# Kernel tuning notes

Measured on AMD Instinct MI355X. Metric: run time of the kernel, lower is better.

Reference implementation:

```python
import jax, jax.numpy as jnp
import numpy as np

N = 100000
E = 1600000
IN_CH = 32
HID = 64
HEADS = 2
NUM_CLASSES = 12
NEG_SLOPE = 0.2


def gat_conv(x, src, dst, W, a_src, a_dst, bias, concat):
    """PyG-style GATConv (self-loops already appended to src/dst).
    x: [N, F_in], W: [F_in, H*C], a_src/a_dst: [H, C], bias: [H*C] or [C]."""
    n = x.shape[0]
    h = (x @ W).reshape(n, HEADS, -1)                    # [N, H, C]
    al_s = jnp.einsum('nhc,hc->nh', h, a_src)            # [N, H]
    al_d = jnp.einsum('nhc,hc->nh', h, a_dst)            # [N, H]
    e = jax.nn.leaky_relu(al_s[src] + al_d[dst], NEG_SLOPE)  # [Etot, H]
    # segment softmax over destination neighborhoods
    e_max = jax.ops.segment_max(e, dst, num_segments=n)      # [N, H]
    ex = jnp.exp(e - e_max[dst])                              # [Etot, H]
    denom = jax.ops.segment_sum(ex, dst, num_segments=n)     # [N, H]
    alpha = ex / denom[dst]                                   # [Etot, H]
    msg = h[src] * alpha[:, :, None]                          # [Etot, H, C]
    out = jax.ops.segment_sum(msg, dst, num_segments=n)      # [N, H, C]
    if concat:
        out = out.reshape(n, -1)
    else:
        out = out.mean(axis=1)
    return out + bias


def prelu(x, a):
    return jnp.where(x >= 0, x, a * x)


def setup_inputs() -> dict:
    key = jax.random.key(0)
    ks = jax.random.split(key, 16)
    HC = HEADS * HID
    d = {
        'x': jax.random.normal(ks[0], (N, IN_CH), jnp.float32),
        'edge_index': jax.random.randint(ks[1], (2, E), 0, N, jnp.int32),
        'W1': jax.random.normal(ks[2], (IN_CH, HC), jnp.float32) * 0.1,
        'a1s': jax.random.normal(ks[3], (HEADS, HID), jnp.float32) * 0.1,
        'a1d': jax.random.normal(ks[4], (HEADS, HID), jnp.float32) * 0.1,
        'b1': jnp.zeros((HC,), jnp.float32),
        'W2': jax.random.normal(ks[5], (HC, HC), jnp.float32) * 0.1,
        'a2s': jax.random.normal(ks[6], (HEADS, HID), jnp.float32) * 0.1,
        'a2d': jax.random.normal(ks[7], (HEADS, HID), jnp.float32) * 0.1,
        'b2': jnp.zeros((HC,), jnp.float32),
        'W3': jax.random.normal(ks[8], (HC, HC), jnp.float32) * 0.1,
        'a3s': jax.random.normal(ks[9], (HEADS, HID), jnp.float32) * 0.1,
        'a3d': jax.random.normal(ks[10], (HEADS, HID), jnp.float32) * 0.1,
        'b3': jnp.zeros((HID,), jnp.float32),
        'prelu_a': jnp.float32(0.25),
        'Wc': jax.random.normal(ks[11], (HID, NUM_CLASSES), jnp.float32) * 0.1,
        'bc': jnp.zeros((NUM_CLASSES,), jnp.float32),
    }
    return d


def reference(x, edge_index, W1, a1s, a1d, b1, W2, a2s, a2d, b2,
              W3, a3s, a3d, b3, prelu_a, Wc, bc):
    loops = jnp.arange(N, dtype=edge_index.dtype)
    src = jnp.concatenate([edge_index[0], loops])
    dst = jnp.concatenate([edge_index[1], loops])
    h = gat_conv(x, src, dst, W1, a1s, a1d, b1, concat=True)
    h = prelu(h, prelu_a)
    h = gat_conv(h, src, dst, W2, a2s, a2d, b2, concat=True)
    h = prelu(h, prelu_a)
    h = gat_conv(h, src, dst, W3, a3s, a3d, b3, concat=False)
    h = prelu(h, prelu_a)
    return h @ Wc + bc
```

## Files before the change

### kernel.cpp

```cpp
#include <hip/hip_runtime.h>
#include <stdint.h>

#define NN 100000
#define NE 1600000
#define ET (NE + NN)
#define HC 128
#define HID 64
#define NCLS 12
#define BSZ 512
#define NBK ((NN + BSZ - 1) / BSZ)
#define CHUNK 8192
#define NPB ((ET + CHUNK - 1) / CHUNK)

typedef _Float16 f16;
typedef _Float16 f16x2 __attribute__((ext_vector_type(2)));
typedef _Float16 f16x4 __attribute__((ext_vector_type(4)));
typedef _Float16 f16x8 __attribute__((ext_vector_type(8)));
typedef float f32x4 __attribute__((ext_vector_type(4)));

__global__ __launch_bounds__(256) void k_hist(const int* __restrict__ ei, int* __restrict__ hgrid) {
    __shared__ int h[NBK];
    int tid = threadIdx.x;
    for (int b = tid; b < NBK; b += 256) h[b] = 0;
    __syncthreads();
    long base = (long)blockIdx.x * CHUNK;
#pragma unroll
    for (int k = 0; k < CHUNK / 256; k++) {
        long i = base + k * 256 + tid;
        if (i < ET) {
            int d = (i < NE) ? ei[NE + i] : (int)(i - NE);
            atomicAdd(&h[d >> 9], 1);
        }
    }
    __syncthreads();
    for (int b = tid; b < NBK; b += 256) hgrid[blockIdx.x * NBK + b] = h[b];
}

__global__ __launch_bounds__(256) void k_bscan(int* __restrict__ hgrid,
                                               int* __restrict__ bucketStart,
                                               int* __restrict__ rp) {
    __shared__ int s[256];
    int tid = threadIdx.x;
    int tot = 0;
    if (tid < NBK)
        for (int b = 0; b < NPB; b++) tot += hgrid[b * NBK + tid];
    s[tid] = tot;
    __syncthreads();
    for (int o = 1; o < 256; o <<= 1) {
        int t = (tid >= o) ? s[tid - o] : 0;
        __syncthreads();
        s[tid] += t;
        __syncthreads();
    }
    int excl = s[tid] - tot;
    if (tid < NBK) {
        bucketStart[tid] = excl;
        int run = excl;
        for (int b = 0; b < NPB; b++) {
            int t = hgrid[b * NBK + tid];
            hgrid[b * NBK + tid] = run;
            run += t;
        }
    }
    if (tid == 0) { bucketStart[NBK] = ET; rp[NN] = ET; }
}

__global__ __launch_bounds__(256) void k_part(const int* __restrict__ ei,
                                              const int* __restrict__ hgrid,
                                              uint32_t* __restrict__ ebuf) {
    __shared__ int h[NBK];
    __shared__ int base[NBK];
    int tid = threadIdx.x;
    for (int b = tid; b < NBK; b += 256) {
        base[b] = hgrid[blockIdx.x * NBK + b];
        h[b] = 0;
    }
    __syncthreads();
    long cbase = (long)blockIdx.x * CHUNK;
#pragma unroll
    for (int k = 0; k < CHUNK / 256; k++) {
        long i = cbase + k * 256 + tid;
        if (i < ET) {
            int s, d;
            if (i < NE) { s = ei[i]; d = ei[NE + i]; } else { s = d = (int)(i - NE); }
            int bk = d >> 9;
            int off = atomicAdd(&h[bk], 1);
            ebuf[base[bk] + off] = (uint32_t)s | ((uint32_t)(d & 511) << 17);
        }
    }
}

__global__ __launch_bounds__(512) void k_build(const uint32_t* __restrict__ ebuf,
                                               const int* __restrict__ bucketStart,
                                               int* __restrict__ rp, int* __restrict__ colx) {
    __shared__ int cnt[BSZ];
    __shared__ int fill[BSZ];
    int b = blockIdx.x, tid = threadIdx.x;
    int e0 = bucketStart[b], e1 = bucketStart[b + 1], m = e1 - e0;
    cnt[tid] = 0;
    __syncthreads();
    for (int k = tid; k < m; k += 512) atomicAdd(&cnt[ebuf[e0 + k] >> 17], 1);
    __syncthreads();
    int v = cnt[tid];
    __syncthreads();
    cnt[tid] = v;
    __syncthreads();
    for (int o = 1; o < 512; o <<= 1) {
        int t = (tid >= o) ? cnt[tid - o] : 0;
        __syncthreads();
        cnt[tid] += t;
        __syncthreads();
    }
    int excl = cnt[tid] - v;
    int node = b * BSZ + tid;
    if (node < NN) rp[node] = e0 + excl;
    fill[tid] = e0 + excl;
    __syncthreads();
    for (int k = tid; k < m; k += 512) {
        uint32_t e = ebuf[e0 + k];
        int pos = atomicAdd(&fill[e >> 17], 1);
        colx[pos] = (int)(e & 0x1FFFF);
    }
}

__global__ void k_wt(const float* __restrict__ W2, const float* __restrict__ W3,
                     f16* __restrict__ wout) {
    int layer = blockIdx.x >> 4, lb = blockIdx.x & 15;
    const float* W = layer ? W3 : W2;
    f16* hi = wout + (size_t)layer * 2 * 2048 * 8;
    f16* lo = hi + 2048 * 8;
    for (int s = lb * 128 + threadIdx.x; s < (lb + 1) * 128; s += 256) {
        int kk = s >> 9, nt = (s >> 6) & 7, l = s & 63;
        int n = nt * 16 + (l & 15), k0 = kk * 32 + (l >> 4) * 8;
        f16x8 vh, vl;
#pragma unroll
        for (int j = 0; j < 8; j++) {
            float v = W[(long)(k0 + j) * HC + n];
            f16 h = (f16)v;
            vh[j] = h;
            vl[j] = (f16)(v - (float)h);
        }
        *(f16x8*)(hi + (size_t)s * 8) = vh;
        *(f16x8*)(lo + (size_t)s * 8) = vl;
    }
}

__global__ __launch_bounds__(256) void k_att1(const float* __restrict__ x,
                                              const float* __restrict__ W1,
                                              const float* __restrict__ a1s,
                                              const float* __restrict__ a1d,
                                              f16* __restrict__ x16,
                                              float* __restrict__ als, float* __restrict__ ald) {
    __shared__ float sIn[128 * 33];
    __shared__ float spv[128];
    int t = threadIdx.x;
    long n0 = (long)blockIdx.x * 128;
    if (t < 128) {
        int sd = t >> 6, h = (t >> 5) & 1, f = t & 31;
        const float* a = sd ? a1d : a1s;
        float acc = 0.f;
        for (int c = 0; c < 64; c++) acc = fmaf(W1[f * HC + h * 64 + c], a[h * 64 + c], acc);
        spv[t] = acc;
    }
    for (int c = t; c < 128 * 8; c += 256) {
        int row = c >> 3, col = (c & 7) * 4;
        long gn = n0 + row;
        if (gn < NN) {
            float4 v = *(const float4*)(x + gn * 32 + col);
            float* dst = &sIn[row * 33 + col];
            dst[0] = v.x; dst[1] = v.y; dst[2] = v.z; dst[3] = v.w;
            f16x4 o;
            o[0] = (f16)v.x; o[1] = (f16)v.y; o[2] = (f16)v.z; o[3] = (f16)v.w;
            *(f16x4*)(x16 + gn * 32 + col) = o;
        }
    }
    __syncthreads();
    int n = t >> 1, h = t & 1;
    long gn = n0 + n;
    if (gn >= NN) return;
    const float* row = &sIn[n * 33];
    const float* as_ = &spv[h * 32];
    const float* ad_ = &spv[64 + h * 32];
    float s_ = 0.f, d_ = 0.f;
#pragma unroll
    for (int f = 0; f < 32; f++) {
        float v = row[f];
        s_ = fmaf(v, as_[f], s_);
        d_ = fmaf(v, ad_[f], d_);
    }
    als[2 * gn + h] = s_;
    ald[2 * gn + h] = d_;
}

__global__ __launch_bounds__(256) void k_aggx(const int* __restrict__ rp, const int* __restrict__ colx,
                                              const f16* __restrict__ x16,
                                              const float* __restrict__ als, const float* __restrict__ ald,
                                              f16* __restrict__ xbar) {
    int wid = blockIdx.x * 4 + (threadIdx.x >> 6);
    int lane = threadIdx.x & 63;
    int g = lane >> 4, li = lane & 15;
    int start = rp[wid], end = rp[wid + 1];
    float2 adv = *(const float2*)(ald + 2 * wid);
    float a00 = 0.f, a01 = 0.f, a10 = 0.f, a11 = 0.f, ws0 = 0.f, ws1 = 0.f;
#pragma unroll 4
    for (int j0 = start; j0 < end; j0 += 4) {
        int j = j0 + g;
        int jc = j < end ? j : end - 1;
        int s = colx[jc];
        float2 asv = *(const float2*)(als + 2 * s);
        float e0 = asv.x + adv.x, e1 = asv.y + adv.y;
        e0 = fmaxf(e0, 0.2f * e0);
        e1 = fmaxf(e1, 0.2f * e1);
        float w0 = __expf(e0), w1 = __expf(e1);
        if (j >= end) { w0 = 0.f; w1 = 0.f; }
        ws0 += w0; ws1 += w1;
        f16x2 xv = *(const f16x2*)(x16 + (long)s * 32 + li * 2);
        float f0 = (float)xv[0], f1 = (float)xv[1];
        a00 = fmaf(w0, f0, a00); a01 = fmaf(w0, f1, a01);
        a10 = fmaf(w1, f0, a10); a11 = fmaf(w1, f1, a11);
    }
#pragma unroll
    for (int o = 16; o <= 32; o <<= 1) {
        ws0 += __shfl_xor(ws0, o); ws1 += __shfl_xor(ws1, o);
        a00 += __shfl_xor(a00, o); a01 += __shfl_xor(a01, o);
        a10 += __shfl_xor(a10, o); a11 += __shfl_xor(a11, o);
    }
    if (g == 0) {
        float inv = 1.0f / ws0;
        f16x2 o; o[0] = (f16)(a00 * inv); o[1] = (f16)(a01 * inv);
        *(f16x2*)(xbar + (long)wid * 64 + li * 2) = o;
    } else if (g == 1) {
        float inv = 1.0f / ws1;
        f16x2 o; o[0] = (f16)(a10 * inv); o[1] = (f16)(a11 * inv);
        *(f16x2*)(xbar + (long)wid * 64 + 32 + li * 2) = o;
    }
}

__global__ __launch_bounds__(256) void k_post1(const f16* __restrict__ xb,
                                               const float* __restrict__ W1,
                                               const float* __restrict__ b1,
                                               const float* __restrict__ pap,
                                               f16* __restrict__ outp) {
    __shared__ __align__(16) float sIn[64 * 64];
    __shared__ __align__(16) float sW[32 * HC];
    __shared__ float sB[HC];
    int tid = threadIdx.x;
    long n0 = (long)blockIdx.x * 64;
    for (int c = tid; c < 64 * 8; c += 256) {
        int row = c >> 3, col = (c & 7) * 8;
        long gn = n0 + row;
        f16x8 v = {};
        if (gn < NN) v = *(const f16x8*)(xb + gn * 64 + col);
#pragma unroll
        for (int j = 0; j < 8; j++) sIn[row * 64 + col + j] = (float)v[j];
    }
    for (int c = tid; c < 32 * HC / 4; c += 256) ((float4*)sW)[c] = ((const float4*)W1)[c];
    if (tid < HC) sB[tid] = b1[tid];
    __syncthreads();
    int cg = tid & 31, ng = tid >> 5, head = cg >> 4;
    float4 acc[8];
#pragma unroll
    for (int i = 0; i < 8; i++) acc[i] = make_float4(0.f, 0.f, 0.f, 0.f);
    for (int k = 0; k < 32; k++) {
        float4 w = *(const float4*)(sW + k * HC + cg * 4);
#pragma unroll
        for (int i = 0; i < 8; i++) {
            float a = sIn[(ng * 8 + i) * 64 + head * 32 + k];
            acc[i].x = fmaf(a, w.x, acc[i].x);
            acc[i].y = fmaf(a, w.y, acc[i].y);
            acc[i].z = fmaf(a, w.z, acc[i].z);
            acc[i].w = fmaf(a, w.w, acc[i].w);
        }
    }
    float pa = pap[0];
    float4 b = *(const float4*)(sB + cg * 4);
#pragma unroll
    for (int i = 0; i < 8; i++) {
        long n = n0 + ng * 8 + i;
        if (n < NN) {
            float o0 = acc[i].x + b.x, o1 = acc[i].y + b.y;
            float o2 = acc[i].z + b.z, o3 = acc[i].w + b.w;
            o0 = o0 >= 0.f ? o0 : pa * o0;
            o1 = o1 >= 0.f ? o1 : pa * o1;
            o2 = o2 >= 0.f ? o2 : pa * o2;
            o3 = o3 >= 0.f ? o3 : pa * o3;
            f16x4 o; o[0] = (f16)o0; o[1] = (f16)o1; o[2] = (f16)o2; o[3] = (f16)o3;
            *(f16x4*)(outp + n * HC + cg * 4) = o;
        }
    }
}

__global__ __launch_bounds__(256) void k_gemmM(const f16* __restrict__ in16,
                                               const f16* __restrict__ wfrag,
                                               const float* __restrict__ avs,
                                               const float* __restrict__ avd,
                                               f16* __restrict__ h16,
                                               float* __restrict__ als, float* __restrict__ ald) {
    const f16* whi = wfrag;
    const f16* wlo = wfrag + 2048 * 8;
    int tid = threadIdx.x;
    int w = tid >> 6, l = tid & 63, q = l >> 4, m = l & 15;
    long n0 = (long)blockIdx.x * 64;
    long rowg = n0 + w * 16 + m;
    bool rok = rowg < NN;
    f32x4 acc[8];
#pragma unroll
    for (int i = 0; i < 8; i++) acc[i] = (f32x4){0.f, 0.f, 0.f, 0.f};
#pragma unroll
    for (int kk = 0; kk < 4; kk++) {
        f16x8 a = {};
        if (rok) a = *(const f16x8*)(in16 + rowg * HC + kk * 32 + q * 8);
#pragma unroll
        for (int nt = 0; nt < 8; nt++) {
            f16x8 bh = *(const f16x8*)(whi + ((kk * 8 + nt) * 64 + l) * 8);
            f16x8 bl = *(const f16x8*)(wlo + ((kk * 8 + nt) * 64 + l) * 8);
            acc[nt] = __builtin_amdgcn_mfma_f32_16x16x32_f16(a, bh, acc[nt], 0, 0, 0);
            acc[nt] = __builtin_amdgcn_mfma_f32_16x16x32_f16(a, bl, acc[nt], 0, 0, 0);
        }
    }
    float as_[8], ad_[8];
#pragma unroll
    for (int nt = 0; nt < 8; nt++) { as_[nt] = avs[nt * 16 + m]; ad_[nt] = avd[nt * 16 + m]; }
#pragma unroll
    for (int r = 0; r < 4; r++) {
        long rg = n0 + w * 16 + q * 4 + r;
        bool ok = rg < NN;
        float s0 = 0.f, s1 = 0.f, d0 = 0.f, d1 = 0.f;
#pragma unroll
        for (int nt = 0; nt < 4; nt++) {
            float v = acc[nt][r];
            s0 = fmaf(v, as_[nt], s0); d0 = fmaf(v, ad_[nt], d0);
        }
#pragma unroll
        for (int nt = 4; nt < 8; nt++) {
            float v = acc[nt][r];
            s1 = fmaf(v, as_[nt], s1); d1 = fmaf(v, ad_[nt], d1);
        }
        if (ok) {
#pragma unroll
            for (int nt = 0; nt < 8; nt++) h16[rg * HC + nt * 16 + m] = (f16)acc[nt][r];
        }
#pragma unroll
        for (int o = 1; o <= 8; o <<= 1) {
            s0 += __shfl_xor(s0, o); s1 += __shfl_xor(s1, o);
            d0 += __shfl_xor(d0, o); d1 += __shfl_xor(d1, o);
        }
        if (ok && m == 0) {
            als[2 * rg] = s0; als[2 * rg + 1] = s1;
            ald[2 * rg] = d0; ald[2 * rg + 1] = d1;
        }
    }
}

template <int MEAN>
__global__ __launch_bounds__(256) void k_agg(const int* __restrict__ rp, const int* __restrict__ colx,
                                             const f16* __restrict__ h,
                                             const float* __restrict__ als, const float* __restrict__ ald,
                                             const float* __restrict__ bias,
                                             const float* __restrict__ pap,
                                             f16* __restrict__ out16) {
    int wid = blockIdx.x * 4 + (threadIdx.x >> 6);
    int lane = threadIdx.x & 63;
    int g = lane >> 4, li = lane & 15;
    int start = rp[wid], end = rp[wid + 1];
    float2 adv = *(const float2*)(ald + 2 * wid);
    float acc[8];
#pragma unroll
    for (int k = 0; k < 8; k++) acc[k] = 0.f;
    float ws0 = 0.f, ws1 = 0.f;
    bool head1 = li >= 8;
#pragma unroll 4
    for (int j0 = start; j0 < end; j0 += 4) {
        int j = j0 + g;
        int jc = j < end ? j : end - 1;
        int s = colx[jc];
        float2 asv = *(const float2*)(als + 2 * s);
        float e0 = asv.x + adv.x, e1 = asv.y + adv.y;
        e0 = fmaxf(e0, 0.2f * e0);
        e1 = fmaxf(e1, 0.2f * e1);
        float w0 = __expf(e0), w1 = __expf(e1);
        if (j >= end) { w0 = 0.f; w1 = 0.f; }
        ws0 += w0; ws1 += w1;
        f16x8 hv = *(const f16x8*)(h + (long)s * HC + li * 8);
        float wsel = head1 ? w1 : w0;
#pragma unroll
        for (int k = 0; k < 8; k++) acc[k] = fmaf(wsel, (float)hv[k], acc[k]);
    }
#pragma unroll
    for (int o = 16; o <= 32; o <<= 1) {
        ws0 += __shfl_xor(ws0, o);
        ws1 += __shfl_xor(ws1, o);
#pragma unroll
        for (int k = 0; k < 8; k++) acc[k] += __shfl_xor(acc[k], o);
    }
    float pa = pap[0];
    if (!MEAN) {
        float inv = 1.0f / (head1 ? ws1 : ws0);
        int c = li * 8 + g * 2;
        float2 bu = *(const float2*)(bias + c);
        float o0 = acc[g * 2] * inv + bu.x;
        float o1 = acc[g * 2 + 1] * inv + bu.y;
        o0 = o0 >= 0.f ? o0 : pa * o0;
        o1 = o1 >= 0.f ? o1 : pa * o1;
        f16x2 o; o[0] = (f16)o0; o[1] = (f16)o1;
        *(f16x2*)(out16 + (long)wid * HC + c) = o;
    } else {
        float inv = 1.0f / (head1 ? ws1 : ws0);
        float v0 = acc[g * 2] * inv, v1 = acc[g * 2 + 1] * inv;
        float p0 = __shfl_xor(v0, 8), p1 = __shfl_xor(v1, 8);
        if (!head1) {
            int c = li * 8 + g * 2;
            float2 bu = *(const float2*)(bias + c);
            float o0 = 0.5f * (v0 + p0) + bu.x;
            float o1 = 0.5f * (v1 + p1) + bu.y;
            o0 = o0 >= 0.f ? o0 : pa * o0;
            o1 = o1 >= 0.f ? o1 : pa * o1;
            f16x2 o; o[0] = (f16)o0; o[1] = (f16)o1;
            *(f16x2*)(out16 + (long)wid * HID + c) = o;
        }
    }
}

__global__ __launch_bounds__(256) void k_cls(const f16* __restrict__ hin,
                                             const float* __restrict__ Wc,
                                             const float* __restrict__ bcp,
                                             float* __restrict__ outp) {
    __shared__ float sW[HID * NCLS];
    __shared__ float sb[NCLS];
    int tid = threadIdx.x;
    for (int c = tid; c < HID * NCLS; c += 256) sW[c] = Wc[c];
    if (tid < NCLS) sb[tid] = bcp[tid];
    __syncthreads();
    int n = blockIdx.x * 256 + tid;
    if (n >= NN) return;
    float o[NCLS];
#pragma unroll
    for (int k = 0; k < NCLS; k++) o[k] = sb[k];
    const f16x8* row = (const f16x8*)(hin + (long)n * HID);
#pragma unroll
    for (int cc = 0; cc < 8; cc++) {
        f16x8 rv = row[cc];
#pragma unroll
        for (int j = 0; j < 8; j++) {
            float v = (float)rv[j];
            int c = cc * 8 + j;
#pragma unroll
            for (int k = 0; k < NCLS; k++) o[k] = fmaf(v, sW[c * NCLS + k], o[k]);
        }
    }
#pragma unroll
    for (int k = 0; k < NCLS; k += 2)
        *(float2*)(outp + (long)n * NCLS + k) = make_float2(o[k], o[k + 1]);
}

extern "C" void kernel_launch(void* const* d_in, const int* in_sizes, int n_in,
                              void* d_out, int out_size, void* d_ws, size_t ws_size,
                              hipStream_t stream) {
    const float* x   = (const float*)d_in[0];
    const int*   ei  = (const int*)d_in[1];
    const float* W1  = (const float*)d_in[2];
    const float* a1s = (const float*)d_in[3];
    const float* a1d = (const float*)d_in[4];
    const float* b1  = (const float*)d_in[5];
    const float* W2  = (const float*)d_in[6];
    const float* a2s = (const float*)d_in[7];
    const float* a2d = (const float*)d_in[8];
    const float* b2  = (const float*)d_in[9];
    const float* W3  = (const float*)d_in[10];
    const float* a3s = (const float*)d_in[11];
    const float* a3d = (const float*)d_in[12];
    const float* b3  = (const float*)d_in[13];
    const float* pa  = (const float*)d_in[14];
    const float* Wc  = (const float*)d_in[15];
    const float* bc  = (const float*)d_in[16];
    float* out = (float*)d_out;

    char* w = (char*)d_ws;
    size_t off = 0;
    auto take = [&](size_t b) { void* p = w + off; off += (b + 255) & ~(size_t)255; return p; };
    int* rp      = (int*)take((size_t)(NN + 1) * 4);
    int* colx    = (int*)take((size_t)ET * 4);
    int* hgrid   = (int*)take((size_t)NPB * NBK * 4);
    int* bstart  = (int*)take((size_t)(NBK + 1) * 4);
    float* als   = (float*)take((size_t)NN * 8);
    float* ald   = (float*)take((size_t)NN * 8);
    f16* wfrag   = (f16*)take((size_t)2 * 2 * 2048 * 8 * 2);
    f16* x16     = (f16*)take((size_t)NN * 32 * 2);
    f16* h16     = (f16*)take((size_t)NN * HC * 2);
    f16* g16     = (f16*)take((size_t)NN * HC * 2);
    f16* xbar    = (f16*)take((size_t)NN * 64 * 2);
    f16* mean16  = (f16*)take((size_t)NN * HID * 2);
    uint32_t* ebuf = (uint32_t*)h16;

    int nb = (NN + 255) / 256;
    int gb = (NN + 63) / 64;
    int ab = NN / 4;
    int tb = (NN + 127) / 128;

    k_hist<<<NPB, 256, 0, stream>>>(ei, hgrid);
    k_bscan<<<1, 256, 0, stream>>>(hgrid, bstart, rp);
    k_part<<<NPB, 256, 0, stream>>>(ei, hgrid, ebuf);
    k_build<<<NBK, 512, 0, stream>>>(ebuf, bstart, rp, colx);
    k_wt<<<32, 256, 0, stream>>>(W2, W3, wfrag);

    k_att1<<<tb, 256, 0, stream>>>(x, W1, a1s, a1d, x16, als, ald);
    k_aggx<<<ab, 256, 0, stream>>>(rp, colx, x16, als, ald, xbar);
    k_post1<<<gb, 256, 0, stream>>>(xbar, W1, b1, pa, g16);
    k_gemmM<<<gb, 256, 0, stream>>>(g16, wfrag, a2s, a2d, h16, als, ald);
    k_agg<0><<<ab, 256, 0, stream>>>(rp, colx, h16, als, ald, b2, pa, g16);
    k_gemmM<<<gb, 256, 0, stream>>>(g16, wfrag + (size_t)2 * 2048 * 8, a3s, a3d, h16, als, ald);
    k_agg<1><<<ab, 256, 0, stream>>>(rp, colx, h16, als, ald, b3, pa, mean16);
    k_cls<<<nb, 256, 0, stream>>>(mean16, Wc, bc, out);
}
```

Before: 430.7 us.

## Slice node features into column-major chunks so aggregation gathers hit a smaller working set

Stores the per-node feature matrices (x16, h16, and the layer-3 output) as slices of 16 channels each, laid out as separate contiguous arrays. The aggregation kernels now launch one block group per slice, each gathering 32-byte rows from a 3.2 MB slice, so the random neighbour gathers should fit better in cache. Layer-3 head averaging, bias and PReLU move into the classifier kernel. The cost is re-reading colx and the attention scores once per slice (8x for the hidden layers) and smaller per-lane loads.

```diff
diff --git a/kernel.cpp b/kernel.cpp
--- a/kernel.cpp
+++ b/kernel.cpp
@@ -149,7 +149,7 @@
                                               const float* __restrict__ W1,
                                               const float* __restrict__ a1s,
                                               const float* __restrict__ a1d,
-                                              f16* __restrict__ x16,
+                                              f16* __restrict__ xT,
                                               float* __restrict__ als, float* __restrict__ ald) {
     __shared__ float sIn[128 * 33];
     __shared__ float spv[128];
@@ -171,7 +171,7 @@
             dst[0] = v.x; dst[1] = v.y; dst[2] = v.z; dst[3] = v.w;
             f16x4 o;
             o[0] = (f16)v.x; o[1] = (f16)v.y; o[2] = (f16)v.z; o[3] = (f16)v.w;
-            *(f16x4*)(x16 + gn * 32 + col) = o;
+            *(f16x4*)(xT + (size_t)(col >> 4) * (NN * 16) + gn * 16 + (col & 15)) = o;
         }
     }
     __syncthreads();
@@ -193,20 +193,22 @@
 }
 
 __global__ __launch_bounds__(256) void k_aggx(const int* __restrict__ rp, const int* __restrict__ colx,
-                                              const f16* __restrict__ x16,
+                                              const f16* __restrict__ xT,
                                               const float* __restrict__ als, const float* __restrict__ ald,
                                               f16* __restrict__ xbar) {
-    int wid = blockIdx.x * 4 + (threadIdx.x >> 6);
+    int slice = blockIdx.x & 1;
+    int wid = (blockIdx.x >> 1) * 4 + (threadIdx.x >> 6);
     int lane = threadIdx.x & 63;
-    int g = lane >> 4, li = lane & 15;
+    int g = lane >> 3, li = lane & 7;
     int start = rp[wid], end = rp[wid + 1];
     float2 adv = *(const float2*)(ald + 2 * wid);
+    const f16* xs = xT + (size_t)slice * (NN * 16);
     float a00 = 0.f, a01 = 0.f, a10 = 0.f, a11 = 0.f, ws0 = 0.f, ws1 = 0.f;
-#pragma unroll 4
-    for (int j0 = start; j0 < end; j0 += 4) {
+#pragma unroll 2
+    for (int j0 = start; j0 < end; j0 += 8) {
         int j = j0 + g;
         int jc = j < end ? j : end - 1;
-        int s = colx[jc];
+        int s = __builtin_nontemporal_load(colx + jc);
         float2 asv = *(const float2*)(als + 2 * s);
         float e0 = asv.x + adv.x, e1 = asv.y + adv.y;
         e0 = fmaxf(e0, 0.2f * e0);
@@ -214,13 +216,13 @@
         float w0 = __expf(e0), w1 = __expf(e1);
         if (j >= end) { w0 = 0.f; w1 = 0.f; }
         ws0 += w0; ws1 += w1;
-        f16x2 xv = *(const f16x2*)(x16 + (long)s * 32 + li * 2);
+        f16x2 xv = *(const f16x2*)(xs + (size_t)s * 16 + li * 2);
         float f0 = (float)xv[0], f1 = (float)xv[1];
         a00 = fmaf(w0, f0, a00); a01 = fmaf(w0, f1, a01);
         a10 = fmaf(w1, f0, a10); a11 = fmaf(w1, f1, a11);
     }
 #pragma unroll
-    for (int o = 16; o <= 32; o <<= 1) {
+    for (int o = 8; o <= 32; o <<= 1) {
         ws0 += __shfl_xor(ws0, o); ws1 += __shfl_xor(ws1, o);
         a00 += __shfl_xor(a00, o); a01 += __shfl_xor(a01, o);
         a10 += __shfl_xor(a10, o); a11 += __shfl_xor(a11, o);
@@ -228,11 +230,11 @@
     if (g == 0) {
         float inv = 1.0f / ws0;
         f16x2 o; o[0] = (f16)(a00 * inv); o[1] = (f16)(a01 * inv);
-        *(f16x2*)(xbar + (long)wid * 64 + li * 2) = o;
+        *(f16x2*)(xbar + (size_t)wid * 64 + slice * 16 + li * 2) = o;
     } else if (g == 1) {
         float inv = 1.0f / ws1;
         f16x2 o; o[0] = (f16)(a10 * inv); o[1] = (f16)(a11 * inv);
-        *(f16x2*)(xbar + (long)wid * 64 + 32 + li * 2) = o;
+        *(f16x2*)(xbar + (size_t)wid * 64 + 32 + slice * 16 + li * 2) = o;
     }
 }
 
@@ -294,7 +296,7 @@
                                                const f16* __restrict__ wfrag,
                                                const float* __restrict__ avs,
                                                const float* __restrict__ avd,
-                                               f16* __restrict__ h16,
+                                               f16* __restrict__ hT,
                                                float* __restrict__ als, float* __restrict__ ald) {
     const f16* whi = wfrag;
     const f16* wlo = wfrag + 2048 * 8;
@@ -338,7 +340,8 @@
         }
         if (ok) {
 #pragma unroll
-            for (int nt = 0; nt < 8; nt++) h16[rg * HC + nt * 16 + m] = (f16)acc[nt][r];
+            for (int nt = 0; nt < 8; nt++)
+                hT[(size_t)nt * (NN * 16) + rg * 16 + m] = (f16)acc[nt][r];
         }
 #pragma unroll
         for (int o = 1; o <= 8; o <<= 1) {
@@ -354,96 +357,98 @@
 
 template <int MEAN>
 __global__ __launch_bounds__(256) void k_agg(const int* __restrict__ rp, const int* __restrict__ colx,
-                                             const f16* __restrict__ h,
+                                             const f16* __restrict__ hT,
                                              const float* __restrict__ als, const float* __restrict__ ald,
                                              const float* __restrict__ bias,
                                              const float* __restrict__ pap,
-                                             f16* __restrict__ out16) {
-    int wid = blockIdx.x * 4 + (threadIdx.x >> 6);
+                                             f16* __restrict__ outp) {
+    int slice = blockIdx.x & 7;
+    int head = slice >> 2;
+    int wid = (blockIdx.x >> 3) * 4 + (threadIdx.x >> 6);
     int lane = threadIdx.x & 63;
-    int g = lane >> 4, li = lane & 15;
+    int g = lane >> 3, li = lane & 7;
     int start = rp[wid], end = rp[wid + 1];
-    float2 adv = *(const float2*)(ald + 2 * wid);
-    float acc[8];
-#pragma unroll
-    for (int k = 0; k < 8; k++) acc[k] = 0.f;
-    float ws0 = 0.f, ws1 = 0.f;
-    bool head1 = li >= 8;
-#pragma unroll 4
-    for (int j0 = start; j0 < end; j0 += 4) {
+    float advh = ald[2 * wid + head];
+    const f16* hs = hT + (size_t)slice * (NN * 16);
+    float a0 = 0.f, a1 = 0.f, ws = 0.f;
+#pragma unroll 2
+    for (int j0 = start; j0 < end; j0 += 8) {
         int j = j0 + g;
         int jc = j < end ? j : end - 1;
-        int s = colx[jc];
-        float2 asv = *(const float2*)(als + 2 * s);
-        float e0 = asv.x + adv.x, e1 = asv.y + adv.y;
-        e0 = fmaxf(e0, 0.2f * e0);
-        e1 = fmaxf(e1, 0.2f * e1);
-        float w0 = __expf(e0), w1 = __expf(e1);
-        if (j >= end) { w0 = 0.f; w1 = 0.f; }
-        ws0 += w0; ws1 += w1;
-        f16x8 hv = *(const f16x8*)(h + (long)s * HC + li * 8);
-        float wsel = head1 ? w1 : w0;
-#pragma unroll
-        for (int k = 0; k < 8; k++) acc[k] = fmaf(wsel, (float)hv[k], acc[k]);
-    }
-#pragma unroll
-    for (int o = 16; o <= 32; o <<= 1) {
-        ws0 += __shfl_xor(ws0, o);
-        ws1 += __shfl_xor(ws1, o);
-#pragma unroll
-        for (int k = 0; k < 8; k++) acc[k] += __shfl_xor(acc[k], o);
-    }
-    float pa = pap[0];
-    if (!MEAN) {
-        float inv = 1.0f / (head1 ? ws1 : ws0);
-        int c = li * 8 + g * 2;
-        float2 bu = *(const float2*)(bias + c);
-        float o0 = acc[g * 2] * inv + bu.x;
-        float o1 = acc[g * 2 + 1] * inv + bu.y;
-        o0 = o0 >= 0.f ? o0 : pa * o0;
-        o1 = o1 >= 0.f ? o1 : pa * o1;
-        f16x2 o; o[0] = (f16)o0; o[1] = (f16)o1;
-        *(f16x2*)(out16 + (long)wid * HC + c) = o;
-    } else {
-        float inv = 1.0f / (head1 ? ws1 : ws0);
-        float v0 = acc[g * 2] * inv, v1 = acc[g * 2 + 1] * inv;
-        float p0 = __shfl_xor(v0, 8), p1 = __shfl_xor(v1, 8);
-        if (!head1) {
-            int c = li * 8 + g * 2;
+        int s = __builtin_nontemporal_load(colx + jc);
+        float e = als[2 * s + head] + advh;
+        e = fmaxf(e, 0.2f * e);
+        float w = __expf(e);
+        if (j >= end) w = 0.f;
+        ws += w;
+        f16x2 hv = *(const f16x2*)(hs + (size_t)s * 16 + li * 2);
+        a0 = fmaf(w, (float)hv[0], a0);
+        a1 = fmaf(w, (float)hv[1], a1);
+    }
+#pragma unroll
+    for (int o = 8; o <= 32; o <<= 1) {
+        ws += __shfl_xor(ws, o);
+        a0 += __shfl_xor(a0, o);
+        a1 += __shfl_xor(a1, o);
+    }
+    if (g == 0) {
+        float inv = 1.0f / ws;
+        if (!MEAN) {
+            int c = slice * 16 + li * 2;
             float2 bu = *(const float2*)(bias + c);
-            float o0 = 0.5f * (v0 + p0) + bu.x;
-            float o1 = 0.5f * (v1 + p1) + bu.y;
+            float pa = pap[0];
+            float o0 = a0 * inv + bu.x;
+            float o1 = a1 * inv + bu.y;
             o0 = o0 >= 0.f ? o0 : pa * o0;
             o1 = o1 >= 0.f ? o1 : pa * o1;
             f16x2 o; o[0] = (f16)o0; o[1] = (f16)o1;
-            *(f16x2*)(out16 + (long)wid * HID + c) = o;
-        }
-    }
-}
-
-__global__ __launch_bounds__(256) void k_cls(const f16* __restrict__ hin,
+            *(f16x2*)(outp + (size_t)wid * HC + c) = o;
+        } else {
+            f16x2 o; o[0] = (f16)(a0 * inv); o[1] = (f16)(a1 * inv);
+            *(f16x2*)(outp + (size_t)slice * (NN * 16) + (size_t)wid * 16 + li * 2) = o;
+        }
+    }
+}
+
+__global__ __launch_bounds__(256) void k_cls(const f16* __restrict__ mT,
                                              const float* __restrict__ Wc,
                                              const float* __restrict__ bcp,
+                                             const float* __restrict__ b3,
+                                             const float* __restrict__ pap,
                                              float* __restrict__ outp) {
     __shared__ float sW[HID * NCLS];
     __shared__ float sb[NCLS];
+    __shared__ float sb3[HID];
     int tid = threadIdx.x;
     for (int c = tid; c < HID * NCLS; c += 256) sW[c] = Wc[c];
     if (tid < NCLS) sb[tid] = bcp[tid];
+    if (tid < HID) sb3[tid] = b3[tid];
     __syncthreads();
     int n = blockIdx.x * 256 + tid;
     if (n >= NN) return;
+    float pa = pap[0];
     float o[NCLS];
 #pragma unroll
     for (int k = 0; k < NCLS; k++) o[k] = sb[k];
-    const f16x8* row = (const f16x8*)(hin + (long)n * HID);
-#pragma unroll
-    for (int cc = 0; cc < 8; cc++) {
-        f16x8 rv = row[cc];
+#pragma unroll
+    for (int sl = 0; sl < 4; sl++) {
+        const f16x8* p0 = (const f16x8*)(mT + (size_t)sl * (NN * 16) + (size_t)n * 16);
+        const f16x8* p1 = (const f16x8*)(mT + (size_t)(sl + 4) * (NN * 16) + (size_t)n * 16);
+        f16x8 q0a = p0[0], q0b = p0[1];
+        f16x8 q1a = p1[0], q1b = p1[1];
 #pragma unroll
         for (int j = 0; j < 8; j++) {
-            float v = (float)rv[j];
-            int c = cc * 8 + j;
+            int c = sl * 16 + j;
+            float v = 0.5f * ((float)q0a[j] + (float)q1a[j]) + sb3[c];
+            v = v >= 0.f ? v : pa * v;
+#pragma unroll
+            for (int k = 0; k < NCLS; k++) o[k] = fmaf(v, sW[c * NCLS + k], o[k]);
+        }
+#pragma unroll
+        for (int j = 0; j < 8; j++) {
+            int c = sl * 16 + 8 + j;
+            float v = 0.5f * ((float)q0b[j] + (float)q1b[j]) + sb3[c];
+            v = v >= 0.f ? v : pa * v;
 #pragma unroll
             for (int k = 0; k < NCLS; k++) o[k] = fmaf(v, sW[c * NCLS + k], o[k]);
         }
@@ -485,16 +490,17 @@
     float* als   = (float*)take((size_t)NN * 8);
     float* ald   = (float*)take((size_t)NN * 8);
     f16* wfrag   = (f16*)take((size_t)2 * 2 * 2048 * 8 * 2);
-    f16* x16     = (f16*)take((size_t)NN * 32 * 2);
-    f16* h16     = (f16*)take((size_t)NN * HC * 2);
+    f16* xT      = (f16*)take((size_t)NN * 32 * 2);
+    f16* hT      = (f16*)take((size_t)NN * HC * 2);
     f16* g16     = (f16*)take((size_t)NN * HC * 2);
     f16* xbar    = (f16*)take((size_t)NN * 64 * 2);
-    f16* mean16  = (f16*)take((size_t)NN * HID * 2);
-    uint32_t* ebuf = (uint32_t*)h16;
+    f16* mT      = (f16*)take((size_t)NN * HC * 2);
+    uint32_t* ebuf = (uint32_t*)hT;
 
     int nb = (NN + 255) / 256;
     int gb = (NN + 63) / 64;
-    int ab = NN / 4;
+    int agb = 8 * (NN / 4);
+    int axb = 2 * (NN / 4);
     int tb = (NN + 127) / 128;
 
     k_hist<<<NPB, 256, 0, stream>>>(ei, hgrid);
@@ -503,12 +509,12 @@
     k_build<<<NBK, 512, 0, stream>>>(ebuf, bstart, rp, colx);
     k_wt<<<32, 256, 0, stream>>>(W2, W3, wfrag);
 
-    k_att1<<<tb, 256, 0, stream>>>(x, W1, a1s, a1d, x16, als, ald);
-    k_aggx<<<ab, 256, 0, stream>>>(rp, colx, x16, als, ald, xbar);
+    k_att1<<<tb, 256, 0, stream>>>(x, W1, a1s, a1d, xT, als, ald);
+    k_aggx<<<axb, 256, 0, stream>>>(rp, colx, xT, als, ald, xbar);
     k_post1<<<gb, 256, 0, stream>>>(xbar, W1, b1, pa, g16);
-    k_gemmM<<<gb, 256, 0, stream>>>(g16, wfrag, a2s, a2d, h16, als, ald);
-    k_agg<0><<<ab, 256, 0, stream>>>(rp, colx, h16, als, ald, b2, pa, g16);
-    k_gemmM<<<gb, 256, 0, stream>>>(g16, wfrag + (size_t)2 * 2048 * 8, a3s, a3d, h16, als, ald);
-    k_agg<1><<<ab, 256, 0, stream>>>(rp, colx, h16, als, ald, b3, pa, mean16);
-    k_cls<<<nb, 256, 0, stream>>>(mean16, Wc, bc, out);
-}
+    k_gemmM<<<gb, 256, 0, stream>>>(g16, wfrag, a2s, a2d, hT, als, ald);
+    k_agg<0><<<agb, 256, 0, stream>>>(rp, colx, hT, als, ald, b2, pa, g16);
+    k_gemmM<<<gb, 256, 0, stream>>>(g16, wfrag + (size_t)2 * 2048 * 8, a3s, a3d, hT, als, ald);
+    k_agg<1><<<agb, 256, 0, stream>>>(rp, colx, hT, als, ald, b3, pa, mT);
+    k_cls<<<nb, 256, 0, stream>>>(mT, Wc, bc, b3, pa, out);
+}
```

Measured after the change: 877.4 us. 2.04x slower.
